# Performance work log

Measured on AMD Instinct MI355X. Metric: run time of the kernel, lower is better.

Reference implementation:

```python
import jax, jax.numpy as jnp
import numpy as np
import math

DIM = 256
NUM_HEADS = 8
WS = 7  # window side (7x7 windows)


def setup_inputs() -> dict:
    key = jax.random.key(0)
    ks = jax.random.split(key, 7)
    B, H, W, C = 32, 56, 56, DIM
    x = jax.random.normal(ks[0], (B, H, W, C), dtype=jnp.float32)
    s = 1.0 / math.sqrt(C)
    Wq = jax.random.normal(ks[1], (C, C), dtype=jnp.float32) * s
    bq = jax.random.normal(ks[2], (C,), dtype=jnp.float32) * 0.01
    Wk = jax.random.normal(ks[3], (C, C), dtype=jnp.float32) * s
    bk = jax.random.normal(ks[4], (C,), dtype=jnp.float32) * 0.01
    Wv = jax.random.normal(ks[5], (C, C), dtype=jnp.float32) * s
    bv = jax.random.normal(ks[6], (C,), dtype=jnp.float32) * 0.01
    return {"x": x, "Wq": Wq, "bq": bq, "Wk": Wk, "bk": bk, "Wv": Wv, "bv": bv}


def _window_partition(x):
    # [B, H, W, C] -> [B, nW, WS*WS, C]
    B, H, W, C = x.shape
    x = x.reshape(B, H // WS, WS, W // WS, WS, C)
    x = x.transpose(0, 1, 3, 2, 4, 5)
    return x.reshape(B, (H // WS) * (W // WS), WS * WS, C)


def reference(x, Wq, bq, Wk, bk, Wv, bv):
    B, H, W, C = x.shape
    hd = C // NUM_HEADS
    win = _window_partition(x)              # [B, nW, T, C], T = 49
    nW, T = win.shape[1], win.shape[2]

    def proj(Wm, bm):
        # nn.Linear: y = x @ W^T + b; split heads -> [B, nW, T, h, hd]
        y = jnp.einsum('bwtc,dc->bwtd', win, Wm) + bm
        return y.reshape(B, nW, T, NUM_HEADS, hd)

    q = proj(Wq, bq)
    k = proj(Wk, bk)
    v = proj(Wv, bv)

    # NOTE: original scales by sqrt(self.dimension) (full dim), not head_dim.
    scale = 1.0 / math.sqrt(C)
    logits = jnp.einsum('bwqhd,bwkhd->bwhqk', q, k) * scale  # [B, nW, h, T, T]
    attn = jax.nn.softmax(logits, axis=-1)
    out = jnp.einsum('bwhqk,bwkhd->bwqhd', attn, v)          # [B, nW, T, h, hd]
    return out.reshape(B, nW, T, C)
```

## Files before the change

kernel.cpp:

```cpp
#include <hip/hip_runtime.h>
#include <hip/hip_bf16.h>

typedef __bf16 bf16_t;
typedef __bf16 bf16x4 __attribute__((ext_vector_type(4)));
typedef __bf16 bf16x8 __attribute__((ext_vector_type(8)));
typedef float  f32x4  __attribute__((ext_vector_type(4)));

#define XP 264
#define QP 72
#define VP 72
#define PP 72
#define SCL 0.09016844f

__device__ inline bf16x8 cvt8(f32x4 a, f32x4 b) {
    bf16x8 r;
    r[0]=(bf16_t)a[0]; r[1]=(bf16_t)a[1]; r[2]=(bf16_t)a[2]; r[3]=(bf16_t)a[3];
    r[4]=(bf16_t)b[0]; r[5]=(bf16_t)b[1]; r[6]=(bf16_t)b[2]; r[7]=(bf16_t)b[3];
    return r;
}

__global__ __launch_bounds__(256)
void wcvt_kernel(const float* __restrict__ Wq, const float* __restrict__ Wk,
                 const float* __restrict__ Wv, bf16_t* __restrict__ o)
{
    int e = (blockIdx.x * 256 + threadIdx.x) * 8;
    const float* src = (e < 65536) ? (Wq + e)
                     : (e < 131072 ? (Wk + (e - 65536)) : (Wv + (e - 131072)));
    f32x4 f0 = *(const f32x4*)src;
    f32x4 f1 = *(const f32x4*)(src + 4);
    *(bf16x8*)(o + e) = cvt8(f0, f1);
}

__global__ __launch_bounds__(256, 3)
void swin_win_attn(const float* __restrict__ x,
                   const bf16_t* __restrict__ Wb,
                   const float* __restrict__ bq, const float* __restrict__ bk,
                   const float* __restrict__ bv,
                   float* __restrict__ out)
{
    __shared__ __attribute__((aligned(16))) bf16_t smem[49 * XP + 2 * 64 * QP + 64 * VP];
    bf16_t* sX  = smem;
    bf16_t* sQ  = smem + 49 * XP;
    bf16_t* sK  = sQ + 64 * QP;
    bf16_t* sVT = sK + 64 * QP;

    const int tid  = threadIdx.x;
    const int wv   = tid >> 6;
    const int lane = tid & 63;
    const int l15  = lane & 15;
    const int quad = lane >> 4;

    const int bid = blockIdx.x;
    const int win = ((bid >> 5) << 3) | (bid & 7);
    const int g   = (bid >> 3) & 3;

    const int b  = win >> 6;
    const int w  = win & 63;
    const int wy = w >> 3;
    const int wx = w & 7;
    const float* xw = x + (((b * 56) + wy * 7) * 56 + wx * 7) * 256;

    f32x4 la[7], lb[7];
    #pragma unroll
    for (int k = 0; k < 6; ++k) {
        int idx = k * 256 + tid, row = idx >> 5, cv = idx & 31;
        int ty = row / 7, tx = row - ty * 7;
        const float* src = xw + (ty * 56 + tx) * 256 + cv * 8;
        la[k] = *(const f32x4*)src;
        lb[k] = *(const f32x4*)(src + 4);
    }
    if (tid < 32) {
        const float* src = xw + (6 * 56 + 6) * 256 + tid * 8;
        la[6] = *(const f32x4*)src;
        lb[6] = *(const f32x4*)(src + 4);
    }
    #pragma unroll
    for (int k = 0; k < 6; ++k) {
        int idx = k * 256 + tid, row = idx >> 5, cv = idx & 31;
        *(bf16x8*)&sX[row * XP + cv * 8] = cvt8(la[k], lb[k]);
    }
    if (tid < 32)
        *(bf16x8*)&sX[48 * XP + tid * 8] = cvt8(la[6], lb[6]);

    const int dglob = g * 64 + wv * 16 + l15;
    const bf16_t* wbase = Wb + dglob * 256 + quad * 8;
    bf16x8 wq[8], wk[8], wvv[8];
    #pragma unroll
    for (int ks = 0; ks < 8; ++ks) {
        wq [ks] = *(const bf16x8*)(wbase + ks * 32);
        wk [ks] = *(const bf16x8*)(wbase + 65536 + ks * 32);
        wvv[ks] = *(const bf16x8*)(wbase + 131072 + ks * 32);
    }
    f32x4 qb4 = *(const f32x4*)&bq[g * 64 + wv * 16 + quad * 4];
    f32x4 kb4 = *(const f32x4*)&bk[g * 64 + wv * 16 + quad * 4];
    const float bvs = bv[dglob];
    __syncthreads();

    f32x4 accq[4], acck[4], accv[4];
    #pragma unroll
    for (int mt = 0; mt < 4; ++mt) {
        accq[mt] = f32x4{0.f,0.f,0.f,0.f};
        acck[mt] = f32x4{0.f,0.f,0.f,0.f};
        accv[mt] = f32x4{0.f,0.f,0.f,0.f};
    }
    #pragma unroll
    for (int ks = 0; ks < 8; ++ks) {
        #pragma unroll
        for (int mt = 0; mt < 4; ++mt) {
            bf16x8 a = *(const bf16x8*)&sX[(mt * 16 + l15) * XP + ks * 32 + quad * 8];
            accq[mt] = __builtin_amdgcn_mfma_f32_16x16x32_bf16(wq [ks], a, accq[mt], 0, 0, 0);
            acck[mt] = __builtin_amdgcn_mfma_f32_16x16x32_bf16(wk [ks], a, acck[mt], 0, 0, 0);
            accv[mt] = __builtin_amdgcn_mfma_f32_16x16x32_bf16(a, wvv[ks], accv[mt], 0, 0, 0);
        }
    }
    #pragma unroll
    for (int mt = 0; mt < 4; ++mt) {
        bf16x4 pq, pk, pv;
        #pragma unroll
        for (int r = 0; r < 4; ++r) {
            pq[r] = (bf16_t)(accq[mt][r] + qb4[r]);
            pk[r] = (bf16_t)(acck[mt][r] + kb4[r]);
            int tok = mt * 16 + quad * 4 + r;
            pv[r] = (tok < 49) ? (bf16_t)(accv[mt][r] + bvs) : (bf16_t)0.0f;
        }
        *(bf16x4*)&sQ [(mt * 16 + l15) * QP + wv * 16 + quad * 4] = pq;
        *(bf16x4*)&sK [(mt * 16 + l15) * QP + wv * 16 + quad * 4] = pk;
        *(bf16x4*)&sVT[(wv * 16 + l15) * VP + mt * 16 + quad * 4] = pv;
    }
    __syncthreads();

    bf16_t* sP = &sX[wv * 16 * PP];
    bf16x8 vone;
    #pragma unroll
    for (int j = 0; j < 8; ++j) vone[j] = (bf16_t)1.0f;

    #pragma unroll
    for (int hs = 0; hs < 2; ++hs) {
        const int hc = hs * 32;
        bf16x8 aq = *(const bf16x8*)&sQ[(wv * 16 + l15) * QP + hc + quad * 8];
        f32x4 sc[4];
        #pragma unroll
        for (int tj = 0; tj < 4; ++tj) {
            bf16x8 kf = *(const bf16x8*)&sK[(tj * 16 + l15) * QP + hc + quad * 8];
            f32x4 z = {0.f, 0.f, 0.f, 0.f};
            sc[tj] = __builtin_amdgcn_mfma_f32_16x16x32_bf16(kf, aq, z, 0, 0, 0);
        }
        #pragma unroll
        for (int tj = 0; tj < 3; ++tj) {
            bf16x4 pp;
            #pragma unroll
            for (int r = 0; r < 4; ++r)
                pp[r] = (bf16_t)__builtin_amdgcn_exp2f(sc[tj][r] * SCL);
            *(bf16x4*)&sP[l15 * PP + tj * 16 + quad * 4] = pp;
        }
        {
            bf16x4 pp;
            pp[0] = (quad == 0) ? (bf16_t)__builtin_amdgcn_exp2f(sc[3][0] * SCL) : (bf16_t)0.0f;
            pp[1] = (bf16_t)0.0f; pp[2] = (bf16_t)0.0f; pp[3] = (bf16_t)0.0f;
            *(bf16x4*)&sP[l15 * PP + 48 + quad * 4] = pp;
        }
        f32x4 o0 = {0.f,0.f,0.f,0.f}, o1 = {0.f,0.f,0.f,0.f}, lsum = {0.f,0.f,0.f,0.f};
        #pragma unroll
        for (int ks = 0; ks < 2; ++ks) {
            bf16x8 ap = *(const bf16x8*)&sP[l15 * PP + ks * 32 + quad * 8];
            bf16x8 b0 = *(const bf16x8*)&sVT[(hc + l15) * VP + ks * 32 + quad * 8];
            bf16x8 b1 = *(const bf16x8*)&sVT[(hc + 16 + l15) * VP + ks * 32 + quad * 8];
            o0   = __builtin_amdgcn_mfma_f32_16x16x32_bf16(ap, b0,   o0,   0, 0, 0);
            o1   = __builtin_amdgcn_mfma_f32_16x16x32_bf16(ap, b1,   o1,   0, 0, 0);
            lsum = __builtin_amdgcn_mfma_f32_16x16x32_bf16(ap, vone, lsum, 0, 0, 0);
        }
        const int h = g * 2 + hs;
        #pragma unroll
        for (int r = 0; r < 4; ++r) {
            int t = wv * 16 + quad * 4 + r;
            if (t < 49) {
                float rinv = __builtin_amdgcn_rcpf(lsum[r]);
                long off = (long)(win * 49 + t) * 256 + h * 32 + l15;
                out[off]      = o0[r] * rinv;
                out[off + 16] = o1[r] * rinv;
            }
        }
    }
}

extern "C" void kernel_launch(void* const* d_in, const int* in_sizes, int n_in,
                              void* d_out, int out_size, void* d_ws, size_t ws_size,
                              hipStream_t stream) {
    const float* x  = (const float*)d_in[0];
    const float* Wq = (const float*)d_in[1];
    const float* bq = (const float*)d_in[2];
    const float* Wk = (const float*)d_in[3];
    const float* bk = (const float*)d_in[4];
    const float* Wv = (const float*)d_in[5];
    const float* bv = (const float*)d_in[6];
    float* out = (float*)d_out;
    bf16_t* Wb = (bf16_t*)d_ws;
    (void)in_sizes; (void)n_in; (void)out_size; (void)ws_size;

    hipLaunchKernelGGL(wcvt_kernel, dim3(96), dim3(256), 0, stream, Wq, Wk, Wv, Wb);
    hipLaunchKernelGGL(swin_win_attn, dim3(8192), dim3(256), 0, stream,
                       x, Wb, bq, bk, bv, out);
}
```

Baseline: 270.3 us.

## Feed projection MFMAs directly from global x and drop LDS staging of X

The block no longer stages the 49x256 window of x in LDS. Each wave now loads its fp32 x fragments straight from global memory, converts them to bf16 in registers and feeds the QKV projection MFMAs, which removes the staging pass and one barrier. The softmax P tile now reuses each wave's own Q rows in LDS after Q is cached in registers. Together these cut LDS use enough to raise the launch-bounds occupancy target from 3 to 4 blocks. The cost is that every wave re-reads the full window from L1/L2, multiplying cache traffic, and global load latency now sits directly in the MFMA loop.

```diff
diff --git a/kernel.cpp b/kernel.cpp
--- a/kernel.cpp
+++ b/kernel.cpp
@@ -6,10 +6,7 @@
 typedef __bf16 bf16x8 __attribute__((ext_vector_type(8)));
 typedef float  f32x4  __attribute__((ext_vector_type(4)));
 
-#define XP 264
 #define QP 72
-#define VP 72
-#define PP 72
 #define SCL 0.09016844f
 
 __device__ inline bf16x8 cvt8(f32x4 a, f32x4 b) {
@@ -31,18 +28,17 @@
     *(bf16x8*)(o + e) = cvt8(f0, f1);
 }
 
-__global__ __launch_bounds__(256, 3)
+__global__ __launch_bounds__(256, 4)
 void swin_win_attn(const float* __restrict__ x,
                    const bf16_t* __restrict__ Wb,
                    const float* __restrict__ bq, const float* __restrict__ bk,
                    const float* __restrict__ bv,
                    float* __restrict__ out)
 {
-    __shared__ __attribute__((aligned(16))) bf16_t smem[49 * XP + 2 * 64 * QP + 64 * VP];
-    bf16_t* sX  = smem;
-    bf16_t* sQ  = smem + 49 * XP;
-    bf16_t* sK  = sQ + 64 * QP;
-    bf16_t* sVT = sK + 64 * QP;
+    __shared__ __attribute__((aligned(16))) bf16_t smem[3 * 64 * QP];
+    bf16_t* sQ  = smem;
+    bf16_t* sK  = smem + 64 * QP;
+    bf16_t* sVT = smem + 2 * 64 * QP;
 
     const int tid  = threadIdx.x;
     const int wv   = tid >> 6;
@@ -60,27 +56,14 @@
     const int wx = w & 7;
     const float* xw = x + (((b * 56) + wy * 7) * 56 + wx * 7) * 256;
 
-    f32x4 la[7], lb[7];
+    const float* abase[4];
     #pragma unroll
-    for (int k = 0; k < 6; ++k) {
-        int idx = k * 256 + tid, row = idx >> 5, cv = idx & 31;
-        int ty = row / 7, tx = row - ty * 7;
-        const float* src = xw + (ty * 56 + tx) * 256 + cv * 8;
-        la[k] = *(const f32x4*)src;
-        lb[k] = *(const f32x4*)(src + 4);
+    for (int mt = 0; mt < 4; ++mt) {
+        int t  = mt * 16 + l15;
+        int tc = (t > 48) ? 48 : t;
+        int ty = tc / 7;
+        abase[mt] = xw + (ty * 49 + tc) * 256 + quad * 8;
     }
-    if (tid < 32) {
-        const float* src = xw + (6 * 56 + 6) * 256 + tid * 8;
-        la[6] = *(const f32x4*)src;
-        lb[6] = *(const f32x4*)(src + 4);
-    }
-    #pragma unroll
-    for (int k = 0; k < 6; ++k) {
-        int idx = k * 256 + tid, row = idx >> 5, cv = idx & 31;
-        *(bf16x8*)&sX[row * XP + cv * 8] = cvt8(la[k], lb[k]);
-    }
-    if (tid < 32)
-        *(bf16x8*)&sX[48 * XP + tid * 8] = cvt8(la[6], lb[6]);
 
     const int dglob = g * 64 + wv * 16 + l15;
     const bf16_t* wbase = Wb + dglob * 256 + quad * 8;
@@ -94,7 +77,6 @@
     f32x4 qb4 = *(const f32x4*)&bq[g * 64 + wv * 16 + quad * 4];
     f32x4 kb4 = *(const f32x4*)&bk[g * 64 + wv * 16 + quad * 4];
     const float bvs = bv[dglob];
-    __syncthreads();
 
     f32x4 accq[4], acck[4], accv[4];
     #pragma unroll
@@ -107,7 +89,10 @@
     for (int ks = 0; ks < 8; ++ks) {
         #pragma unroll
         for (int mt = 0; mt < 4; ++mt) {
-            bf16x8 a = *(const bf16x8*)&sX[(mt * 16 + l15) * XP + ks * 32 + quad * 8];
+            const float* p = abase[mt] + ks * 32;
+            f32x4 a0 = *(const f32x4*)p;
+            f32x4 a1 = *(const f32x4*)(p + 4);
+            bf16x8 a = cvt8(a0, a1);
             accq[mt] = __builtin_amdgcn_mfma_f32_16x16x32_bf16(wq [ks], a, accq[mt], 0, 0, 0);
             acck[mt] = __builtin_amdgcn_mfma_f32_16x16x32_bf16(wk [ks], a, acck[mt], 0, 0, 0);
             accv[mt] = __builtin_amdgcn_mfma_f32_16x16x32_bf16(a, wvv[ks], accv[mt], 0, 0, 0);
@@ -125,11 +110,14 @@
         }
         *(bf16x4*)&sQ [(mt * 16 + l15) * QP + wv * 16 + quad * 4] = pq;
         *(bf16x4*)&sK [(mt * 16 + l15) * QP + wv * 16 + quad * 4] = pk;
-        *(bf16x4*)&sVT[(wv * 16 + l15) * VP + mt * 16 + quad * 4] = pv;
+        *(bf16x4*)&sVT[(wv * 16 + l15) * QP + mt * 16 + quad * 4] = pv;
     }
     __syncthreads();
 
-    bf16_t* sP = &sX[wv * 16 * PP];
+    bf16x8 aqh[2];
+    aqh[0] = *(const bf16x8*)&sQ[(wv * 16 + l15) * QP + 0  + quad * 8];
+    aqh[1] = *(const bf16x8*)&sQ[(wv * 16 + l15) * QP + 32 + quad * 8];
+    bf16_t* sP = &sQ[(wv * 16) * QP];
     bf16x8 vone;
     #pragma unroll
     for (int j = 0; j < 8; ++j) vone[j] = (bf16_t)1.0f;
@@ -137,13 +125,12 @@
     #pragma unroll
     for (int hs = 0; hs < 2; ++hs) {
         const int hc = hs * 32;
-        bf16x8 aq = *(const bf16x8*)&sQ[(wv * 16 + l15) * QP + hc + quad * 8];
         f32x4 sc[4];
         #pragma unroll
         for (int tj = 0; tj < 4; ++tj) {
             bf16x8 kf = *(const bf16x8*)&sK[(tj * 16 + l15) * QP + hc + quad * 8];
             f32x4 z = {0.f, 0.f, 0.f, 0.f};
-            sc[tj] = __builtin_amdgcn_mfma_f32_16x16x32_bf16(kf, aq, z, 0, 0, 0);
+            sc[tj] = __builtin_amdgcn_mfma_f32_16x16x32_bf16(kf, aqh[hs], z, 0, 0, 0);
         }
         #pragma unroll
         for (int tj = 0; tj < 3; ++tj) {
@@ -151,20 +138,20 @@
             #pragma unroll
             for (int r = 0; r < 4; ++r)
                 pp[r] = (bf16_t)__builtin_amdgcn_exp2f(sc[tj][r] * SCL);
-            *(bf16x4*)&sP[l15 * PP + tj * 16 + quad * 4] = pp;
+            *(bf16x4*)&sP[l15 * QP + tj * 16 + quad * 4] = pp;
         }
         {
             bf16x4 pp;
             pp[0] = (quad == 0) ? (bf16_t)__builtin_amdgcn_exp2f(sc[3][0] * SCL) : (bf16_t)0.0f;
             pp[1] = (bf16_t)0.0f; pp[2] = (bf16_t)0.0f; pp[3] = (bf16_t)0.0f;
-            *(bf16x4*)&sP[l15 * PP + 48 + quad * 4] = pp;
+            *(bf16x4*)&sP[l15 * QP + 48 + quad * 4] = pp;
         }
         f32x4 o0 = {0.f,0.f,0.f,0.f}, o1 = {0.f,0.f,0.f,0.f}, lsum = {0.f,0.f,0.f,0.f};
         #pragma unroll
         for (int ks = 0; ks < 2; ++ks) {
-            bf16x8 ap = *(const bf16x8*)&sP[l15 * PP + ks * 32 + quad * 8];
-            bf16x8 b0 = *(const bf16x8*)&sVT[(hc + l15) * VP + ks * 32 + quad * 8];
-            bf16x8 b1 = *(const bf16x8*)&sVT[(hc + 16 + l15) * VP + ks * 32 + quad * 8];
+            bf16x8 ap = *(const bf16x8*)&sP[l15 * QP + ks * 32 + quad * 8];
+            bf16x8 b0 = *(const bf16x8*)&sVT[(hc + l15) * QP + ks * 32 + quad * 8];
+            bf16x8 b1 = *(const bf16x8*)&sVT[(hc + 16 + l15) * QP + ks * 32 + quad * 8];
             o0   = __builtin_amdgcn_mfma_f32_16x16x32_bf16(ap, b0,   o0,   0, 0, 0);
             o1   = __builtin_amdgcn_mfma_f32_16x16x32_bf16(ap, b1,   o1,   0, 0, 0);
             lsum = __builtin_amdgcn_mfma_f32_16x16x32_bf16(ap, vone, lsum, 0, 0, 0);
```

Measured after the change: 426.5 us. 57.8% more time.

## Make attention kernel persistent with software-pipelined prefetch of next window

Applied to the files above, without the earlier changes.

Replaces the one-block-per-(window, head-group) grid with a persistent grid of 768 blocks. Each block loads its weight fragments once and loops over 10-11 windows, stepping 192 windows at a time. The next window's x tile is fetched from global memory into registers during the attention phase and written into sX in chunks, overlapping the load with compute. The P buffer is aliased onto sQ so that sX can be refilled early. This amortizes weight loads and hides input latency, at the cost of more register pressure and a serialized per-block loop with fewer blocks in flight.

```diff
diff --git a/kernel.cpp b/kernel.cpp
--- a/kernel.cpp
+++ b/kernel.cpp
@@ -8,8 +8,6 @@
 
 #define XP 264
 #define QP 72
-#define VP 72
-#define PP 72
 #define SCL 0.09016844f
 
 __device__ inline bf16x8 cvt8(f32x4 a, f32x4 b) {
@@ -38,7 +36,7 @@
                    const float* __restrict__ bv,
                    float* __restrict__ out)
 {
-    __shared__ __attribute__((aligned(16))) bf16_t smem[49 * XP + 2 * 64 * QP + 64 * VP];
+    __shared__ __attribute__((aligned(16))) bf16_t smem[49 * XP + 3 * 64 * QP];
     bf16_t* sX  = smem;
     bf16_t* sQ  = smem + 49 * XP;
     bf16_t* sK  = sQ + 64 * QP;
@@ -50,37 +48,10 @@
     const int l15  = lane & 15;
     const int quad = lane >> 4;
 
-    const int bid = blockIdx.x;
-    const int win = ((bid >> 5) << 3) | (bid & 7);
-    const int g   = (bid >> 3) & 3;
-
-    const int b  = win >> 6;
-    const int w  = win & 63;
-    const int wy = w >> 3;
-    const int wx = w & 7;
-    const float* xw = x + (((b * 56) + wy * 7) * 56 + wx * 7) * 256;
-
-    f32x4 la[7], lb[7];
-    #pragma unroll
-    for (int k = 0; k < 6; ++k) {
-        int idx = k * 256 + tid, row = idx >> 5, cv = idx & 31;
-        int ty = row / 7, tx = row - ty * 7;
-        const float* src = xw + (ty * 56 + tx) * 256 + cv * 8;
-        la[k] = *(const f32x4*)src;
-        lb[k] = *(const f32x4*)(src + 4);
-    }
-    if (tid < 32) {
-        const float* src = xw + (6 * 56 + 6) * 256 + tid * 8;
-        la[6] = *(const f32x4*)src;
-        lb[6] = *(const f32x4*)(src + 4);
-    }
-    #pragma unroll
-    for (int k = 0; k < 6; ++k) {
-        int idx = k * 256 + tid, row = idx >> 5, cv = idx & 31;
-        *(bf16x8*)&sX[row * XP + cv * 8] = cvt8(la[k], lb[k]);
-    }
-    if (tid < 32)
-        *(bf16x8*)&sX[48 * XP + tid * 8] = cvt8(la[6], lb[6]);
+    const int bid  = blockIdx.x;
+    const int g    = bid & 3;
+    const int slot = bid >> 2;
+    const int nwin = (slot < 128) ? 11 : 10;
 
     const int dglob = g * 64 + wv * 16 + l15;
     const bf16_t* wbase = Wb + dglob * 256 + quad * 8;
@@ -91,95 +62,233 @@
         wk [ks] = *(const bf16x8*)(wbase + 65536 + ks * 32);
         wvv[ks] = *(const bf16x8*)(wbase + 131072 + ks * 32);
     }
-    f32x4 qb4 = *(const f32x4*)&bq[g * 64 + wv * 16 + quad * 4];
-    f32x4 kb4 = *(const f32x4*)&bk[g * 64 + wv * 16 + quad * 4];
+    const f32x4 qb4 = *(const f32x4*)&bq[g * 64 + wv * 16 + quad * 4];
+    const f32x4 kb4 = *(const f32x4*)&bk[g * 64 + wv * 16 + quad * 4];
     const float bvs = bv[dglob];
-    __syncthreads();
-
-    f32x4 accq[4], acck[4], accv[4];
-    #pragma unroll
-    for (int mt = 0; mt < 4; ++mt) {
-        accq[mt] = f32x4{0.f,0.f,0.f,0.f};
-        acck[mt] = f32x4{0.f,0.f,0.f,0.f};
-        accv[mt] = f32x4{0.f,0.f,0.f,0.f};
-    }
-    #pragma unroll
-    for (int ks = 0; ks < 8; ++ks) {
-        #pragma unroll
-        for (int mt = 0; mt < 4; ++mt) {
-            bf16x8 a = *(const bf16x8*)&sX[(mt * 16 + l15) * XP + ks * 32 + quad * 8];
-            accq[mt] = __builtin_amdgcn_mfma_f32_16x16x32_bf16(wq [ks], a, accq[mt], 0, 0, 0);
-            acck[mt] = __builtin_amdgcn_mfma_f32_16x16x32_bf16(wk [ks], a, acck[mt], 0, 0, 0);
-            accv[mt] = __builtin_amdgcn_mfma_f32_16x16x32_bf16(a, wvv[ks], accv[mt], 0, 0, 0);
-        }
-    }
-    #pragma unroll
-    for (int mt = 0; mt < 4; ++mt) {
-        bf16x4 pq, pk, pv;
-        #pragma unroll
-        for (int r = 0; r < 4; ++r) {
-            pq[r] = (bf16_t)(accq[mt][r] + qb4[r]);
-            pk[r] = (bf16_t)(acck[mt][r] + kb4[r]);
-            int tok = mt * 16 + quad * 4 + r;
-            pv[r] = (tok < 49) ? (bf16_t)(accv[mt][r] + bvs) : (bf16_t)0.0f;
-        }
-        *(bf16x4*)&sQ [(mt * 16 + l15) * QP + wv * 16 + quad * 4] = pq;
-        *(bf16x4*)&sK [(mt * 16 + l15) * QP + wv * 16 + quad * 4] = pk;
-        *(bf16x4*)&sVT[(wv * 16 + l15) * VP + mt * 16 + quad * 4] = pv;
-    }
-    __syncthreads();
-
-    bf16_t* sP = &sX[wv * 16 * PP];
     bf16x8 vone;
     #pragma unroll
     for (int j = 0; j < 8; ++j) vone[j] = (bf16_t)1.0f;
 
-    #pragma unroll
-    for (int hs = 0; hs < 2; ++hs) {
-        const int hc = hs * 32;
-        bf16x8 aq = *(const bf16x8*)&sQ[(wv * 16 + l15) * QP + hc + quad * 8];
-        f32x4 sc[4];
+    {
+        const int w0 = slot, b0 = w0 >> 6, wy0 = (w0 >> 3) & 7, wx0 = w0 & 7;
+        const float* xw = x + (((b0 * 56) + wy0 * 7) * 56 + wx0 * 7) * 256;
+        f32x4 pa[6], pb[6], ra, rb;
         #pragma unroll
-        for (int tj = 0; tj < 4; ++tj) {
-            bf16x8 kf = *(const bf16x8*)&sK[(tj * 16 + l15) * QP + hc + quad * 8];
-            f32x4 z = {0.f, 0.f, 0.f, 0.f};
-            sc[tj] = __builtin_amdgcn_mfma_f32_16x16x32_bf16(kf, aq, z, 0, 0, 0);
+        for (int k = 0; k < 6; ++k) {
+            int idx = k * 256 + tid, row = idx >> 5, cv = idx & 31;
+            int ty = row / 7, tx = row - ty * 7;
+            const float* src = xw + (ty * 56 + tx) * 256 + cv * 8;
+            pa[k] = *(const f32x4*)src;
+            pb[k] = *(const f32x4*)(src + 4);
+        }
+        if (tid < 32) {
+            const float* src = xw + (6 * 56 + 6) * 256 + tid * 8;
+            ra = *(const f32x4*)src; rb = *(const f32x4*)(src + 4);
         }
         #pragma unroll
-        for (int tj = 0; tj < 3; ++tj) {
-            bf16x4 pp;
-            #pragma unroll
-            for (int r = 0; r < 4; ++r)
-                pp[r] = (bf16_t)__builtin_amdgcn_exp2f(sc[tj][r] * SCL);
-            *(bf16x4*)&sP[l15 * PP + tj * 16 + quad * 4] = pp;
-        }
+        for (int k = 0; k < 6; ++k) {
+            int idx = k * 256 + tid, row = idx >> 5, cv = idx & 31;
+            *(bf16x8*)&sX[row * XP + cv * 8] = cvt8(pa[k], pb[k]);
+        }
+        if (tid < 32)
+            *(bf16x8*)&sX[48 * XP + tid * 8] = cvt8(ra, rb);
+    }
+    __syncthreads();
+
+    int w = slot;
+    for (int it = 0; it < nwin; ++it) {
+        const bool more = (it + 1 < nwin);
+        const int wn = w + 192;
+        const float* xwn = x;
+        if (more) {
+            int bn = wn >> 6, wyn = (wn >> 3) & 7, wxn = wn & 7;
+            xwn = x + (((bn * 56) + wyn * 7) * 56 + wxn * 7) * 256;
+        }
+
+        #pragma unroll
+        for (int half = 0; half < 2; ++half) {
+            f32x4 aq[2], ak[2], av[2];
+            #pragma unroll
+            for (int m = 0; m < 2; ++m) {
+                aq[m] = f32x4{0.f,0.f,0.f,0.f};
+                ak[m] = f32x4{0.f,0.f,0.f,0.f};
+                av[m] = f32x4{0.f,0.f,0.f,0.f};
+            }
+            #pragma unroll
+            for (int ks = 0; ks < 8; ++ks) {
+                #pragma unroll
+                for (int m = 0; m < 2; ++m) {
+                    int mt = half * 2 + m;
+                    bf16x8 a = *(const bf16x8*)&sX[(mt * 16 + l15) * XP + ks * 32 + quad * 8];
+                    aq[m] = __builtin_amdgcn_mfma_f32_16x16x32_bf16(wq [ks], a, aq[m], 0, 0, 0);
+                    ak[m] = __builtin_amdgcn_mfma_f32_16x16x32_bf16(wk [ks], a, ak[m], 0, 0, 0);
+                    av[m] = __builtin_amdgcn_mfma_f32_16x16x32_bf16(a, wvv[ks], av[m], 0, 0, 0);
+                }
+            }
+            #pragma unroll
+            for (int m = 0; m < 2; ++m) {
+                int mt = half * 2 + m;
+                bf16x4 pq, pk, pv;
+                #pragma unroll
+                for (int r = 0; r < 4; ++r) {
+                    pq[r] = (bf16_t)(aq[m][r] + qb4[r]);
+                    pk[r] = (bf16_t)(ak[m][r] + kb4[r]);
+                    int tok = mt * 16 + quad * 4 + r;
+                    pv[r] = (tok < 49) ? (bf16_t)(av[m][r] + bvs) : (bf16_t)0.0f;
+                }
+                *(bf16x4*)&sQ [(mt * 16 + l15) * QP + wv * 16 + quad * 4] = pq;
+                *(bf16x4*)&sK [(mt * 16 + l15) * QP + wv * 16 + quad * 4] = pk;
+                *(bf16x4*)&sVT[(wv * 16 + l15) * QP + mt * 16 + quad * 4] = pv;
+            }
+        }
+        __syncthreads();
+
+        bf16x8 aqh0 = *(const bf16x8*)&sQ[(wv * 16 + l15) * QP + 0  + quad * 8];
+        bf16x8 aqh1 = *(const bf16x8*)&sQ[(wv * 16 + l15) * QP + 32 + quad * 8];
+        bf16_t* sP = &sQ[(wv * 16) * QP];
+
+        f32x4 ca0, cb0, ca1, cb1, ra, rb;
+        if (more) {
+            {   int idx = tid,       row = idx >> 5, cv = idx & 31;
+                int ty = row / 7, tx = row - ty * 7;
+                const float* src = xwn + (ty * 56 + tx) * 256 + cv * 8;
+                ca0 = *(const f32x4*)src; cb0 = *(const f32x4*)(src + 4); }
+            {   int idx = 256 + tid, row = idx >> 5, cv = idx & 31;
+                int ty = row / 7, tx = row - ty * 7;
+                const float* src = xwn + (ty * 56 + tx) * 256 + cv * 8;
+                ca1 = *(const f32x4*)src; cb1 = *(const f32x4*)(src + 4); }
+            if (tid < 32) {
+                const float* src = xwn + (6 * 56 + 6) * 256 + tid * 8;
+                ra = *(const f32x4*)src; rb = *(const f32x4*)(src + 4);
+            }
+        }
+
         {
-            bf16x4 pp;
-            pp[0] = (quad == 0) ? (bf16_t)__builtin_amdgcn_exp2f(sc[3][0] * SCL) : (bf16_t)0.0f;
-            pp[1] = (bf16_t)0.0f; pp[2] = (bf16_t)0.0f; pp[3] = (bf16_t)0.0f;
-            *(bf16x4*)&sP[l15 * PP + 48 + quad * 4] = pp;
-        }
-        f32x4 o0 = {0.f,0.f,0.f,0.f}, o1 = {0.f,0.f,0.f,0.f}, lsum = {0.f,0.f,0.f,0.f};
-        #pragma unroll
-        for (int ks = 0; ks < 2; ++ks) {
-            bf16x8 ap = *(const bf16x8*)&sP[l15 * PP + ks * 32 + quad * 8];
-            bf16x8 b0 = *(const bf16x8*)&sVT[(hc + l15) * VP + ks * 32 + quad * 8];
-            bf16x8 b1 = *(const bf16x8*)&sVT[(hc + 16 + l15) * VP + ks * 32 + quad * 8];
-            o0   = __builtin_amdgcn_mfma_f32_16x16x32_bf16(ap, b0,   o0,   0, 0, 0);
-            o1   = __builtin_amdgcn_mfma_f32_16x16x32_bf16(ap, b1,   o1,   0, 0, 0);
-            lsum = __builtin_amdgcn_mfma_f32_16x16x32_bf16(ap, vone, lsum, 0, 0, 0);
-        }
-        const int h = g * 2 + hs;
-        #pragma unroll
-        for (int r = 0; r < 4; ++r) {
-            int t = wv * 16 + quad * 4 + r;
-            if (t < 49) {
-                float rinv = __builtin_amdgcn_rcpf(lsum[r]);
-                long off = (long)(win * 49 + t) * 256 + h * 32 + l15;
-                out[off]      = o0[r] * rinv;
-                out[off + 16] = o1[r] * rinv;
-            }
-        }
+            f32x4 sc[4];
+            #pragma unroll
+            for (int tj = 0; tj < 4; ++tj) {
+                bf16x8 kf = *(const bf16x8*)&sK[(tj * 16 + l15) * QP + 0 + quad * 8];
+                f32x4 z = {0.f, 0.f, 0.f, 0.f};
+                sc[tj] = __builtin_amdgcn_mfma_f32_16x16x32_bf16(kf, aqh0, z, 0, 0, 0);
+            }
+            #pragma unroll
+            for (int tj = 0; tj < 3; ++tj) {
+                bf16x4 pp;
+                #pragma unroll
+                for (int r = 0; r < 4; ++r)
+                    pp[r] = (bf16_t)__builtin_amdgcn_exp2f(sc[tj][r] * SCL);
+                *(bf16x4*)&sP[l15 * QP + tj * 16 + quad * 4] = pp;
+            }
+            {   bf16x4 pp;
+                pp[0] = (quad == 0) ? (bf16_t)__builtin_amdgcn_exp2f(sc[3][0] * SCL) : (bf16_t)0.0f;
+                pp[1] = (bf16_t)0.0f; pp[2] = (bf16_t)0.0f; pp[3] = (bf16_t)0.0f;
+                *(bf16x4*)&sP[l15 * QP + 48 + quad * 4] = pp;
+            }
+            if (more) {
+                {   int idx = tid,       row = idx >> 5, cv = idx & 31;
+                    *(bf16x8*)&sX[row * XP + cv * 8] = cvt8(ca0, cb0); }
+                {   int idx = 256 + tid, row = idx >> 5, cv = idx & 31;
+                    *(bf16x8*)&sX[row * XP + cv * 8] = cvt8(ca1, cb1); }
+                {   int idx = 512 + tid, row = idx >> 5, cv = idx & 31;
+                    int ty = row / 7, tx = row - ty * 7;
+                    const float* src = xwn + (ty * 56 + tx) * 256 + cv * 8;
+                    ca0 = *(const f32x4*)src; cb0 = *(const f32x4*)(src + 4); }
+                {   int idx = 768 + tid, row = idx >> 5, cv = idx & 31;
+                    int ty = row / 7, tx = row - ty * 7;
+                    const float* src = xwn + (ty * 56 + tx) * 256 + cv * 8;
+                    ca1 = *(const f32x4*)src; cb1 = *(const f32x4*)(src + 4); }
+            }
+            f32x4 o0 = {0.f,0.f,0.f,0.f}, o1 = {0.f,0.f,0.f,0.f}, lsum = {0.f,0.f,0.f,0.f};
+            #pragma unroll
+            for (int ks = 0; ks < 2; ++ks) {
+                bf16x8 ap = *(const bf16x8*)&sP[l15 * QP + ks * 32 + quad * 8];
+                bf16x8 b0 = *(const bf16x8*)&sVT[(0  + l15) * QP + ks * 32 + quad * 8];
+                bf16x8 b1 = *(const bf16x8*)&sVT[(16 + l15) * QP + ks * 32 + quad * 8];
+                o0   = __builtin_amdgcn_mfma_f32_16x16x32_bf16(ap, b0,   o0,   0, 0, 0);
+                o1   = __builtin_amdgcn_mfma_f32_16x16x32_bf16(ap, b1,   o1,   0, 0, 0);
+                lsum = __builtin_amdgcn_mfma_f32_16x16x32_bf16(ap, vone, lsum, 0, 0, 0);
+            }
+            const int h = g * 2;
+            #pragma unroll
+            for (int r = 0; r < 4; ++r) {
+                int t = wv * 16 + quad * 4 + r;
+                if (t < 49) {
+                    float rinv = __builtin_amdgcn_rcpf(lsum[r]);
+                    long off = (long)(w * 49 + t) * 256 + h * 32 + l15;
+                    out[off]      = o0[r] * rinv;
+                    out[off + 16] = o1[r] * rinv;
+                }
+            }
+            if (more) {
+                {   int idx = 512 + tid, row = idx >> 5, cv = idx & 31;
+                    *(bf16x8*)&sX[row * XP + cv * 8] = cvt8(ca0, cb0); }
+                {   int idx = 768 + tid, row = idx >> 5, cv = idx & 31;
+                    *(bf16x8*)&sX[row * XP + cv * 8] = cvt8(ca1, cb1); }
+                {   int idx = 1024 + tid, row = idx >> 5, cv = idx & 31;
+                    int ty = row / 7, tx = row - ty * 7;
+                    const float* src = xwn + (ty * 56 + tx) * 256 + cv * 8;
+                    ca0 = *(const f32x4*)src; cb0 = *(const f32x4*)(src + 4); }
+                {   int idx = 1280 + tid, row = idx >> 5, cv = idx & 31;
+                    int ty = row / 7, tx = row - ty * 7;
+                    const float* src = xwn + (ty * 56 + tx) * 256 + cv * 8;
+                    ca1 = *(const f32x4*)src; cb1 = *(const f32x4*)(src + 4); }
+            }
+        }
+
+        {
+            f32x4 sc[4];
+            #pragma unroll
+            for (int tj = 0; tj < 4; ++tj) {
+                bf16x8 kf = *(const bf16x8*)&sK[(tj * 16 + l15) * QP + 32 + quad * 8];
+                f32x4 z = {0.f, 0.f, 0.f, 0.f};
+                sc[tj] = __builtin_amdgcn_mfma_f32_16x16x32_bf16(kf, aqh1, z, 0, 0, 0);
+            }
+            #pragma unroll
+            for (int tj = 0; tj < 3; ++tj) {
+                bf16x4 pp;
+                #pragma unroll
+                for (int r = 0; r < 4; ++r)
+                    pp[r] = (bf16_t)__builtin_amdgcn_exp2f(sc[tj][r] * SCL);
+                *(bf16x4*)&sP[l15 * QP + tj * 16 + quad * 4] = pp;
+            }
+            {   bf16x4 pp;
+                pp[0] = (quad == 0) ? (bf16_t)__builtin_amdgcn_exp2f(sc[3][0] * SCL) : (bf16_t)0.0f;
+                pp[1] = (bf16_t)0.0f; pp[2] = (bf16_t)0.0f; pp[3] = (bf16_t)0.0f;
+                *(bf16x4*)&sP[l15 * QP + 48 + quad * 4] = pp;
+            }
+            if (more) {
+                {   int idx = 1024 + tid, row = idx >> 5, cv = idx & 31;
+                    *(bf16x8*)&sX[row * XP + cv * 8] = cvt8(ca0, cb0); }
+                {   int idx = 1280 + tid, row = idx >> 5, cv = idx & 31;
+                    *(bf16x8*)&sX[row * XP + cv * 8] = cvt8(ca1, cb1); }
+                if (tid < 32)
+                    *(bf16x8*)&sX[48 * XP + tid * 8] = cvt8(ra, rb);
+            }
+            f32x4 o0 = {0.f,0.f,0.f,0.f}, o1 = {0.f,0.f,0.f,0.f}, lsum = {0.f,0.f,0.f,0.f};
+            #pragma unroll
+            for (int ks = 0; ks < 2; ++ks) {
+                bf16x8 ap = *(const bf16x8*)&sP[l15 * QP + ks * 32 + quad * 8];
+                bf16x8 b0 = *(const bf16x8*)&sVT[(32 + l15) * QP + ks * 32 + quad * 8];
+                bf16x8 b1 = *(const bf16x8*)&sVT[(48 + l15) * QP + ks * 32 + quad * 8];
+                o0   = __builtin_amdgcn_mfma_f32_16x16x32_bf16(ap, b0,   o0,   0, 0, 0);
+                o1   = __builtin_amdgcn_mfma_f32_16x16x32_bf16(ap, b1,   o1,   0, 0, 0);
+                lsum = __builtin_amdgcn_mfma_f32_16x16x32_bf16(ap, vone, lsum, 0, 0, 0);
+            }
+            const int h = g * 2 + 1;
+            #pragma unroll
+            for (int r = 0; r < 4; ++r) {
+                int t = wv * 16 + quad * 4 + r;
+                if (t < 49) {
+                    float rinv = __builtin_amdgcn_rcpf(lsum[r]);
+                    long off = (long)(w * 49 + t) * 256 + h * 32 + l15;
+                    out[off]      = o0[r] * rinv;
+                    out[off + 16] = o1[r] * rinv;
+                }
+            }
+        }
+
+        __syncthreads();
+        w = wn;
     }
 }
 
@@ -198,6 +307,6 @@
     (void)in_sizes; (void)n_in; (void)out_size; (void)ws_size;
 
     hipLaunchKernelGGL(wcvt_kernel, dim3(96), dim3(256), 0, stream, Wq, Wk, Wv, Wb);
-    hipLaunchKernelGGL(swin_win_attn, dim3(8192), dim3(256), 0, stream,
+    hipLaunchKernelGGL(swin_win_attn, dim3(768), dim3(256), 0, stream,
                        x, Wb, bq, bk, bv, out);
 }
```

Result: slower. 406.5 us (+50.4%).

## Swizzle LDS layouts and alias Q into X buffer to fit four blocks per CU

Applied to the files above, without the earlier changes.

Replaces the padded LDS row strides with XOR-swizzled unpadded layouts and removes the separate Q buffer. Q tiles are held in registers across a barrier and then written over the dead X region, with P scratch also placed there. This shrinks shared memory per block so the launch bound can be raised from 3 to 4 blocks per CU, aiming at more latency hiding. The cost is an extra barrier, possibly more register pressure under the tighter launch bound, and the K rows past token 49 are no longer written.

```diff
diff --git a/kernel.cpp b/kernel.cpp
--- a/kernel.cpp
+++ b/kernel.cpp
@@ -6,11 +6,10 @@
 typedef __bf16 bf16x8 __attribute__((ext_vector_type(8)));
 typedef float  f32x4  __attribute__((ext_vector_type(4)));
 
-#define XP 264
-#define QP 72
-#define VP 72
-#define PP 72
 #define SCL 0.09016844f
+
+__device__ inline int swzX(int row, int col) { return row * 256 + (col ^ ((row & 7) << 3)); }
+__device__ inline int swz64(int row, int col) { return row * 64  + (col ^ ((row & 7) << 3)); }
 
 __device__ inline bf16x8 cvt8(f32x4 a, f32x4 b) {
     bf16x8 r;
@@ -31,18 +30,17 @@
     *(bf16x8*)(o + e) = cvt8(f0, f1);
 }
 
-__global__ __launch_bounds__(256, 3)
+__global__ __launch_bounds__(256, 4)
 void swin_win_attn(const float* __restrict__ x,
                    const bf16_t* __restrict__ Wb,
                    const float* __restrict__ bq, const float* __restrict__ bk,
                    const float* __restrict__ bv,
                    float* __restrict__ out)
 {
-    __shared__ __attribute__((aligned(16))) bf16_t smem[49 * XP + 2 * 64 * QP + 64 * VP];
+    __shared__ __attribute__((aligned(16))) bf16_t smem[49 * 256 + 49 * 64 + 64 * 64];
     bf16_t* sX  = smem;
-    bf16_t* sQ  = smem + 49 * XP;
-    bf16_t* sK  = sQ + 64 * QP;
-    bf16_t* sVT = sK + 64 * QP;
+    bf16_t* sK  = smem + 12544;
+    bf16_t* sVT = smem + 15680;
 
     const int tid  = threadIdx.x;
     const int wv   = tid >> 6;
@@ -77,10 +75,10 @@
     #pragma unroll
     for (int k = 0; k < 6; ++k) {
         int idx = k * 256 + tid, row = idx >> 5, cv = idx & 31;
-        *(bf16x8*)&sX[row * XP + cv * 8] = cvt8(la[k], lb[k]);
+        *(bf16x8*)&sX[swzX(row, cv * 8)] = cvt8(la[k], lb[k]);
     }
     if (tid < 32)
-        *(bf16x8*)&sX[48 * XP + tid * 8] = cvt8(la[6], lb[6]);
+        *(bf16x8*)&sX[swzX(48, tid * 8)] = cvt8(la[6], lb[6]);
 
     const int dglob = g * 64 + wv * 16 + l15;
     const bf16_t* wbase = Wb + dglob * 256 + quad * 8;
@@ -107,12 +105,13 @@
     for (int ks = 0; ks < 8; ++ks) {
         #pragma unroll
         for (int mt = 0; mt < 4; ++mt) {
-            bf16x8 a = *(const bf16x8*)&sX[(mt * 16 + l15) * XP + ks * 32 + quad * 8];
+            bf16x8 a = *(const bf16x8*)&sX[swzX(mt * 16 + l15, ks * 32 + quad * 8)];
             accq[mt] = __builtin_amdgcn_mfma_f32_16x16x32_bf16(wq [ks], a, accq[mt], 0, 0, 0);
             acck[mt] = __builtin_amdgcn_mfma_f32_16x16x32_bf16(wk [ks], a, acck[mt], 0, 0, 0);
             accv[mt] = __builtin_amdgcn_mfma_f32_16x16x32_bf16(a, wvv[ks], accv[mt], 0, 0, 0);
         }
     }
+    bf16x4 qs0, qs1, qs2, qs3;
     #pragma unroll
     for (int mt = 0; mt < 4; ++mt) {
         bf16x4 pq, pk, pv;
@@ -123,13 +122,23 @@
             int tok = mt * 16 + quad * 4 + r;
             pv[r] = (tok < 49) ? (bf16_t)(accv[mt][r] + bvs) : (bf16_t)0.0f;
         }
-        *(bf16x4*)&sQ [(mt * 16 + l15) * QP + wv * 16 + quad * 4] = pq;
-        *(bf16x4*)&sK [(mt * 16 + l15) * QP + wv * 16 + quad * 4] = pk;
-        *(bf16x4*)&sVT[(wv * 16 + l15) * VP + mt * 16 + quad * 4] = pv;
+        if (mt == 0) qs0 = pq; else if (mt == 1) qs1 = pq;
+        else if (mt == 2) qs2 = pq; else qs3 = pq;
+        if (mt * 16 + l15 < 49)
+            *(bf16x4*)&sK[swz64(mt * 16 + l15, wv * 16 + quad * 4)] = pk;
+        *(bf16x4*)&sVT[swz64(wv * 16 + l15, mt * 16 + quad * 4)] = pv;
     }
     __syncthreads();
 
-    bf16_t* sP = &sX[wv * 16 * PP];
+    *(bf16x4*)&smem[swz64(0 * 16 + l15, wv * 16 + quad * 4)] = qs0;
+    *(bf16x4*)&smem[swz64(1 * 16 + l15, wv * 16 + quad * 4)] = qs1;
+    *(bf16x4*)&smem[swz64(2 * 16 + l15, wv * 16 + quad * 4)] = qs2;
+    *(bf16x4*)&smem[swz64(3 * 16 + l15, wv * 16 + quad * 4)] = qs3;
+    __syncthreads();
+
+    bf16x8 aqh0 = *(const bf16x8*)&smem[swz64(wv * 16 + l15, 0  + quad * 8)];
+    bf16x8 aqh1 = *(const bf16x8*)&smem[swz64(wv * 16 + l15, 32 + quad * 8)];
+    bf16_t* sP = smem + 4096 + wv * 1024;
     bf16x8 vone;
     #pragma unroll
     for (int j = 0; j < 8; ++j) vone[j] = (bf16_t)1.0f;
@@ -137,13 +146,13 @@
     #pragma unroll
     for (int hs = 0; hs < 2; ++hs) {
         const int hc = hs * 32;
-        bf16x8 aq = *(const bf16x8*)&sQ[(wv * 16 + l15) * QP + hc + quad * 8];
+        const bf16x8 aqf = (hs == 0) ? aqh0 : aqh1;
         f32x4 sc[4];
         #pragma unroll
         for (int tj = 0; tj < 4; ++tj) {
-            bf16x8 kf = *(const bf16x8*)&sK[(tj * 16 + l15) * QP + hc + quad * 8];
+            bf16x8 kf = *(const bf16x8*)&sK[swz64(tj * 16 + l15, hc + quad * 8)];
             f32x4 z = {0.f, 0.f, 0.f, 0.f};
-            sc[tj] = __builtin_amdgcn_mfma_f32_16x16x32_bf16(kf, aq, z, 0, 0, 0);
+            sc[tj] = __builtin_amdgcn_mfma_f32_16x16x32_bf16(kf, aqf, z, 0, 0, 0);
         }
         #pragma unroll
         for (int tj = 0; tj < 3; ++tj) {
@@ -151,20 +160,20 @@
             #pragma unroll
             for (int r = 0; r < 4; ++r)
                 pp[r] = (bf16_t)__builtin_amdgcn_exp2f(sc[tj][r] * SCL);
-            *(bf16x4*)&sP[l15 * PP + tj * 16 + quad * 4] = pp;
+            *(bf16x4*)&sP[swz64(l15, tj * 16 + quad * 4)] = pp;
         }
         {
             bf16x4 pp;
             pp[0] = (quad == 0) ? (bf16_t)__builtin_amdgcn_exp2f(sc[3][0] * SCL) : (bf16_t)0.0f;
             pp[1] = (bf16_t)0.0f; pp[2] = (bf16_t)0.0f; pp[3] = (bf16_t)0.0f;
-            *(bf16x4*)&sP[l15 * PP + 48 + quad * 4] = pp;
+            *(bf16x4*)&sP[swz64(l15, 48 + quad * 4)] = pp;
         }
         f32x4 o0 = {0.f,0.f,0.f,0.f}, o1 = {0.f,0.f,0.f,0.f}, lsum = {0.f,0.f,0.f,0.f};
         #pragma unroll
         for (int ks = 0; ks < 2; ++ks) {
-            bf16x8 ap = *(const bf16x8*)&sP[l15 * PP + ks * 32 + quad * 8];
-            bf16x8 b0 = *(const bf16x8*)&sVT[(hc + l15) * VP + ks * 32 + quad * 8];
-            bf16x8 b1 = *(const bf16x8*)&sVT[(hc + 16 + l15) * VP + ks * 32 + quad * 8];
+            bf16x8 ap = *(const bf16x8*)&sP[swz64(l15, ks * 32 + quad * 8)];
+            bf16x8 b0 = *(const bf16x8*)&sVT[swz64(hc + l15,      ks * 32 + quad * 8)];
+            bf16x8 b1 = *(const bf16x8*)&sVT[swz64(hc + 16 + l15, ks * 32 + quad * 8)];
             o0   = __builtin_amdgcn_mfma_f32_16x16x32_bf16(ap, b0,   o0,   0, 0, 0);
             o1   = __builtin_amdgcn_mfma_f32_16x16x32_bf16(ap, b1,   o1,   0, 0, 0);
             lsum = __builtin_amdgcn_mfma_f32_16x16x32_bf16(ap, vone, lsum, 0, 0, 0);
```

Result: slower. 356.7 us (+32.0%).
